# Kernel optimization log

Hardware: AMD Instinct MI355X
Metric: run time of the kernel (lower is better)

The kernel has to match this reference:

```python
import jax, jax.numpy as jnp
import numpy as np

N_NODES = 100000
N_EDGES = 800000
N_DIM = 2
HID = 128
EPS = 1e-12  # torch F.normalize eps


def setup_inputs() -> dict:
    key = jax.random.key(0)
    ks = jax.random.split(key, 12)
    x = jax.random.normal(ks[0], (N_NODES, N_DIM), dtype=jnp.float32)
    v = jax.random.normal(ks[1], (N_NODES, N_DIM), dtype=jnp.float32)
    src = jax.random.randint(ks[2], (N_EDGES,), 0, N_NODES, dtype=jnp.int32)
    dst = jax.random.randint(ks[3], (N_EDGES,), 0, N_NODES, dtype=jnp.int32)
    # fNN parameters, stored as [in, out] (y = h @ W + b, equivalent to torch Linear)
    def lin(k, fan_in, fan_out):
        bound = 1.0 / np.sqrt(fan_in)
        kw, kb = jax.random.split(k)
        W = jax.random.uniform(kw, (fan_in, fan_out), jnp.float32, -bound, bound)
        b = jax.random.uniform(kb, (fan_out,), jnp.float32, -bound, bound)
        return W, b
    W0, b0 = lin(ks[4], 1, HID)
    W1, b1 = lin(ks[5], HID, HID)
    W2, b2 = lin(ks[6], HID, HID)
    W3, b3 = lin(ks[7], HID, 1)
    gamma = jnp.float32(0.1)
    return {"x": x, "v": v, "src": src, "dst": dst, "gamma": gamma,
            "W0": W0, "b0": b0, "W1": W1, "b1": b1,
            "W2": W2, "b2": b2, "W3": W3, "b3": b3}


def reference(x, v, src, dst, gamma, W0, b0, W1, b1, W2, b2, W3, b3):
    n_nodes = x.shape[0]
    # per-edge displacement: dst position - src position (non-periodic euclid)
    dr = x[dst] - x[src]                                  # [E, N_dim]
    abs_dr = jnp.linalg.norm(dr, axis=-1, keepdims=True)  # [E, 1]
    unit_dr = dr / jnp.maximum(abs_dr, EPS)               # F.normalize
    # small MLP on scalar distance: 1 -> 128 -> 128 -> 128 -> 1, ReLU between
    h = jax.nn.relu(abs_dr @ W0 + b0)
    h = jax.nn.relu(h @ W1 + b1)
    h = jax.nn.relu(h @ W2 + b2)
    force = h @ W3 + b3                                   # [E, 1]
    msg = force * unit_dr                                 # [E, N_dim]
    # scatter-sum messages onto destination nodes
    sum_force = jax.ops.segment_sum(msg, dst, num_segments=n_nodes)  # [N, N_dim]
    # acceleration = aggregated force - gamma * velocity
    return sum_force - gamma * v
```

## Files before the change

kernel.cpp:

```cpp
#include <hip/hip_runtime.h>
#include <math.h>


#define M_TAB 4096
#define INV_MTAB (1.0f / 4096.0f)
#define EPSF 1e-12f
#define RANGE_N 2048
#define RSHIFT 11
#define NBUCK 64
#define P_SL 8
#define BCHUNK 2048
#define TPTS 8
#define NTABB (M_TAB / TPTS)
#define MAXRUN 64
#define SRC_BITS 17
#define SRC_MASK 0x1FFFFu

__device__ __forceinline__ void build_table8(
    int base, int tid, const float* __restrict__ W0,
    const float* __restrict__ b0, const float* __restrict__ W1,
    const float* __restrict__ b1, const float* __restrict__ W2,
    const float* __restrict__ b2, const float* __restrict__ W3,
    const float* __restrict__ b3, float* __restrict__ table,
    float* bufA, float* bufB) {
  const int j = tid;
  if (j < 128) {
    float w = W0[j], b = b0[j];
#pragma unroll
    for (int p = 0; p < TPTS; ++p) {
      float u = (float)(base + p) * INV_MTAB;
      float dd = u / (1.f - u);
      bufA[j * TPTS + p] = fmaxf(fmaf(dd, w, b), 0.f);
    }
  }
  __syncthreads();
  float acc[TPTS];
  if (j < 128) {
    float b = b1[j];
#pragma unroll
    for (int p = 0; p < TPTS; ++p) acc[p] = b;
#pragma unroll 8
    for (int k = 0; k < 128; ++k) {
      float w = W1[k * 128 + j];
      float4 h0 = *(const float4*)&bufA[k * TPTS];
      float4 h1 = *(const float4*)&bufA[k * TPTS + 4];
      acc[0] = fmaf(h0.x, w, acc[0]);
      acc[1] = fmaf(h0.y, w, acc[1]);
      acc[2] = fmaf(h0.z, w, acc[2]);
      acc[3] = fmaf(h0.w, w, acc[3]);
      acc[4] = fmaf(h1.x, w, acc[4]);
      acc[5] = fmaf(h1.y, w, acc[5]);
      acc[6] = fmaf(h1.z, w, acc[6]);
      acc[7] = fmaf(h1.w, w, acc[7]);
    }
  }
  __syncthreads();
  if (j < 128) {
#pragma unroll
    for (int p = 0; p < TPTS; ++p) bufB[j * TPTS + p] = fmaxf(acc[p], 0.f);
  }
  __syncthreads();
  if (j < 128) {
    float b = b2[j];
#pragma unroll
    for (int p = 0; p < TPTS; ++p) acc[p] = b;
#pragma unroll 8
    for (int k = 0; k < 128; ++k) {
      float w = W2[k * 128 + j];
      float4 h0 = *(const float4*)&bufB[k * TPTS];
      float4 h1 = *(const float4*)&bufB[k * TPTS + 4];
      acc[0] = fmaf(h0.x, w, acc[0]);
      acc[1] = fmaf(h0.y, w, acc[1]);
      acc[2] = fmaf(h0.z, w, acc[2]);
      acc[3] = fmaf(h0.w, w, acc[3]);
      acc[4] = fmaf(h1.x, w, acc[4]);
      acc[5] = fmaf(h1.y, w, acc[5]);
      acc[6] = fmaf(h1.z, w, acc[6]);
      acc[7] = fmaf(h1.w, w, acc[7]);
    }
    float w3 = W3[j];
#pragma unroll
    for (int p = 0; p < TPTS; ++p) bufA[j * TPTS + p] = fmaxf(acc[p], 0.f) * w3;
  }
  __syncthreads();
  for (int s = 64; s > 0; s >>= 1) {
    if (j < s) {
#pragma unroll
      for (int p = 0; p < TPTS; ++p)
        bufA[j * TPTS + p] += bufA[(j + s) * TPTS + p];
    }
    __syncthreads();
  }
  if (j < TPTS) table[base + j] = bufA[j] + b3[0];
}

__global__ __launch_bounds__(256) void kbin(
    const int* __restrict__ src, const int* __restrict__ dst,
    const float* __restrict__ W0, const float* __restrict__ b0,
    const float* __restrict__ W1, const float* __restrict__ b1,
    const float* __restrict__ W2, const float* __restrict__ b2,
    const float* __restrict__ W3, const float* __restrict__ b3,
    unsigned* __restrict__ binData, int* __restrict__ cntTab,
    int* __restrict__ offTab, float* __restrict__ table, int E, int NB) {
  __shared__ float smem[2048];
  __shared__ int cntL[NBUCK];
  __shared__ int offL[NBUCK];
  const int tid = threadIdx.x;
  const int bid = blockIdx.x;

  if (bid < NTABB) {
    build_table8(bid * TPTS, tid, W0, b0, W1, b1, W2, b2, W3, b3, table,
                 smem, smem + 1024);
    return;
  }
  const int b = bid - NTABB;
  if (tid < NBUCK) cntL[tid] = 0;
  __syncthreads();
  const int e0 = b * BCHUNK + tid * 8;
  int mdst[8], msrc[8], mrank[8];
  if (e0 + 7 < E) {
    int4 c0 = *(const int4*)(dst + e0);
    int4 c1 = *(const int4*)(dst + e0 + 4);
    int4 a0 = *(const int4*)(src + e0);
    int4 a1 = *(const int4*)(src + e0 + 4);
    mdst[0] = c0.x; mdst[1] = c0.y; mdst[2] = c0.z; mdst[3] = c0.w;
    mdst[4] = c1.x; mdst[5] = c1.y; mdst[6] = c1.z; mdst[7] = c1.w;
    msrc[0] = a0.x; msrc[1] = a0.y; msrc[2] = a0.z; msrc[3] = a0.w;
    msrc[4] = a1.x; msrc[5] = a1.y; msrc[6] = a1.z; msrc[7] = a1.w;
  } else {
#pragma unroll
    for (int i = 0; i < 8; ++i) {
      bool vv = (e0 + i < E);
      msrc[i] = vv ? src[e0 + i] : 0;
      mdst[i] = vv ? dst[e0 + i] : -1;
    }
  }
#pragma unroll
  for (int i = 0; i < 8; ++i)
    if (mdst[i] >= 0) mrank[i] = atomicAdd(&cntL[mdst[i] >> RSHIFT], 1);
  __syncthreads();
  if (tid == 0) {
    int s = 0;
#pragma unroll
    for (int k = 0; k < NBUCK; ++k) {
      offL[k] = s;
      s += cntL[k];
    }
  }
  __syncthreads();
  if (tid < NBUCK) {
    cntTab[b * NBUCK + tid] = cntL[tid];
    offTab[b * NBUCK + tid] = offL[tid];
  }
  unsigned* gout = binData + (size_t)b * BCHUNK;
#pragma unroll
  for (int i = 0; i < 8; ++i) {
    if (mdst[i] >= 0) {
      int pos = offL[mdst[i] >> RSHIFT] + mrank[i];
      gout[pos] = ((unsigned)(mdst[i] & (RANGE_N - 1)) << SRC_BITS) |
                  (unsigned)msrc[i];
    }
  }
}

__global__ __launch_bounds__(512) void kcons(
    const unsigned* __restrict__ binData, const int* __restrict__ cntTab,
    const int* __restrict__ offTab, const float* __restrict__ table,
    const float* __restrict__ x, float* __restrict__ partial, int NB,
    int n_nodes, int n_out) {
  __shared__ float acc[RANGE_N * 2];
  __shared__ float2 xl[RANGE_N];
  __shared__ int runStart[MAXRUN];
  __shared__ int pref[MAXRUN + 1];
  const int tid = threadIdx.x;
  const int p = blockIdx.x & (P_SL - 1);
  const int r = blockIdx.x >> 3;
  const int node0 = r * RANGE_N;

  for (int i = tid; i < RANGE_N * 2; i += 512) acc[i] = 0.f;
  for (int i = tid; i < RANGE_N; i += 512)
    xl[i] = (node0 + i < n_nodes) ? ((const float2*)x)[node0 + i]
                                  : make_float2(0.f, 0.f);
  const int nrun = (NB - p + P_SL - 1) / P_SL;
  for (int j = tid; j < nrun; j += 512) {
    int b = p + j * P_SL;
    runStart[j] = b * BCHUNK + offTab[b * NBUCK + r];
    pref[j + 1] = cntTab[b * NBUCK + r];
  }
  __syncthreads();
  if (tid == 0) {
    pref[0] = 0;
    for (int j = 0; j < nrun; ++j) pref[j + 1] += pref[j];
  }
  __syncthreads();

  const int T = pref[nrun];
  for (int g = tid; g < T; g += 512) {
    int lo = 0, hi = nrun;
    while (hi - lo > 1) {
      int mid = (lo + hi) >> 1;
      if (pref[mid] <= g) lo = mid; else hi = mid;
    }
    unsigned ent = binData[(size_t)runStart[lo] + (g - pref[lo])];
    int dloc = (int)(ent >> SRC_BITS);
    int s = (int)(ent & SRC_MASK);
    float2 xs = ((const float2*)x)[s];
    float2 xt = xl[dloc];
    float dx = xt.x - xs.x, dy = xt.y - xs.y;
    float d = sqrtf(fmaf(dx, dx, dy * dy));
    float u = d / (1.f + d);
    float idxf = u * (float)M_TAB;
    int i0 = (int)idxf;
    if (i0 > M_TAB - 2) i0 = M_TAB - 2;
    float frac = idxf - (float)i0;
    float f0 = table[i0], f1 = table[i0 + 1];
    float f = fmaf(frac, f1 - f0, f0);
    float sc = f / fmaxf(d, EPSF);
    atomicAdd(&acc[dloc * 2], sc * dx);
    atomicAdd(&acc[dloc * 2 + 1], sc * dy);
  }
  __syncthreads();

  const int cnt2 = min(RANGE_N, n_nodes - node0);
  float2* po = (float2*)(partial + (size_t)p * n_out) + node0;
  const float2* a2 = (const float2*)acc;
  for (int i = tid; i < cnt2; i += 512) po[i] = a2[i];
}

__global__ __launch_bounds__(256) void k4_finish(
    const float4* __restrict__ v4, const float* __restrict__ gamma,
    const float4* __restrict__ part4, float4* __restrict__ out4, int n4) {
  int i = blockIdx.x * blockDim.x + threadIdx.x;
  if (i >= n4) return;
  float g = -gamma[0];
  float4 a = v4[i];
  float4 acc = make_float4(g * a.x, g * a.y, g * a.z, g * a.w);
#pragma unroll
  for (int c = 0; c < P_SL; ++c) {
    float4 p = part4[(size_t)c * n4 + i];
    acc.x += p.x;
    acc.y += p.y;
    acc.z += p.z;
    acc.w += p.w;
  }
  out4[i] = acc;
}

__global__ __launch_bounds__(128) void k2_table(
    const float* __restrict__ W0, const float* __restrict__ b0,
    const float* __restrict__ W1, const float* __restrict__ b1,
    const float* __restrict__ W2, const float* __restrict__ b2,
    const float* __restrict__ W3, const float* __restrict__ b3,
    float* __restrict__ table) {
  __shared__ float bufA[1024];
  __shared__ float bufB[1024];
  build_table8(blockIdx.x * TPTS, threadIdx.x, W0, b0, W1, b1, W2, b2, W3,
               b3, table, bufA, bufB);
}

__global__ __launch_bounds__(256) void k0_init(const float* __restrict__ v,
                                               const float* __restrict__ gamma,
                                               float* __restrict__ out,
                                               int n) {
  int i = blockIdx.x * blockDim.x + threadIdx.x;
  if (i < n) out[i] = -gamma[0] * v[i];
}

__global__ __launch_bounds__(256) void k3_direct(
    const float* __restrict__ x, const int* __restrict__ src,
    const int* __restrict__ dst, const float* __restrict__ table,
    float* __restrict__ out, int E) {
  int e = blockIdx.x * blockDim.x + threadIdx.x;
  if (e >= E) return;
  int s = src[e], t = dst[e];
  float2 xs = ((const float2*)x)[s];
  float2 xt = ((const float2*)x)[t];
  float dx = xt.x - xs.x, dy = xt.y - xs.y;
  float d = sqrtf(fmaf(dx, dx, dy * dy));
  float u = d / (1.f + d);
  float idxf = u * (float)M_TAB;
  int i0 = (int)idxf;
  if (i0 > M_TAB - 2) i0 = M_TAB - 2;
  float frac = idxf - (float)i0;
  float f = fmaf(frac, table[i0 + 1] - table[i0], table[i0]);
  float sc = f / fmaxf(d, EPSF);
  atomicAdd(&out[2 * t + 0], sc * dx);
  atomicAdd(&out[2 * t + 1], sc * dy);
}

extern "C" void kernel_launch(void* const* d_in, const int* in_sizes, int n_in,
                              void* d_out, int out_size, void* d_ws,
                              size_t ws_size, hipStream_t stream) {
  const float* x = (const float*)d_in[0];
  const float* v = (const float*)d_in[1];
  const int* src = (const int*)d_in[2];
  const int* dst = (const int*)d_in[3];
  const float* gamma = (const float*)d_in[4];
  const float* W0 = (const float*)d_in[5];
  const float* b0 = (const float*)d_in[6];
  const float* W1 = (const float*)d_in[7];
  const float* b1 = (const float*)d_in[8];
  const float* W2 = (const float*)d_in[9];
  const float* b2 = (const float*)d_in[10];
  const float* W3 = (const float*)d_in[11];
  const float* b3 = (const float*)d_in[12];
  float* out = (float*)d_out;
  float* table = (float*)d_ws;

  int n_out = out_size;
  int n_nodes = in_sizes[0] / 2;
  int E = in_sizes[2];

  const int NB = (E + BCHUNK - 1) / BCHUNK;
  const int NR = (n_nodes + RANGE_N - 1) / RANGE_N;
  size_t sz_tab = ((size_t)NB * NBUCK * 4 + 255) & ~(size_t)255;
  size_t off_cnt = 65536;
  size_t off_off = off_cnt + sz_tab;
  size_t off_part = off_off + sz_tab;
  size_t off_bin = off_part + (size_t)P_SL * n_out * 4;
  size_t need = off_bin + (size_t)NB * BCHUNK * 4;

  bool fast = (ws_size >= need) && (n_out == 2 * n_nodes) &&
              (n_nodes <= (1 << SRC_BITS)) && (NR <= NBUCK) &&
              (NB <= P_SL * MAXRUN) && ((n_out & 3) == 0);

  if (fast) {
    int* cntTab = (int*)((char*)d_ws + off_cnt);
    int* offTab = (int*)((char*)d_ws + off_off);
    float* partial = (float*)((char*)d_ws + off_part);
    unsigned* binData = (unsigned*)((char*)d_ws + off_bin);
    hipLaunchKernelGGL(kbin, dim3(NTABB + NB), dim3(256), 0, stream, src, dst,
                       W0, b0, W1, b1, W2, b2, W3, b3, binData, cntTab,
                       offTab, table, E, NB);
    hipLaunchKernelGGL(kcons, dim3(NR * P_SL), dim3(512), 0, stream, binData,
                       cntTab, offTab, table, x, partial, NB, n_nodes, n_out);
    hipLaunchKernelGGL(k4_finish, dim3((n_out / 4 + 255) / 256), dim3(256), 0,
                       stream, (const float4*)v, gamma, (const float4*)partial,
                       (float4*)out, n_out / 4);
  } else {
    hipLaunchKernelGGL(k2_table, dim3(NTABB), dim3(128), 0, stream, W0, b0,
                       W1, b1, W2, b2, W3, b3, table);
    hipLaunchKernelGGL(k0_init, dim3((n_out + 255) / 256), dim3(256), 0,
                       stream, v, gamma, out, n_out);
    hipLaunchKernelGGL(k3_direct, dim3((E + 255) / 256), dim3(256), 0, stream,
                       x, src, dst, table, out, E);
  }
}
```

Before: 42.85 us.

## Use fine-grained node ranges with one consumer block each and fuse finish

Shrinks the destination range per bucket from 2048 to 256 nodes, giving 391 buckets. Each consumer block now owns one range and walks all edge chunks, which removes the 8-way partial slices and lets it write the final output (sum minus gamma times v) directly, so the separate finish kernel and partial buffers go away. Bucket prefix sums in both kernels become a two-level parallel scan to cope with the larger bucket and run counts. The cost is more per-chunk table entries to write and read, and each consumer block scans about 400 runs with a deeper binary search.

```diff
diff --git a/kernel.cpp b/kernel.cpp
--- a/kernel.cpp
+++ b/kernel.cpp
@@ -5,14 +5,13 @@
 #define M_TAB 4096
 #define INV_MTAB (1.0f / 4096.0f)
 #define EPSF 1e-12f
-#define RANGE_N 2048
-#define RSHIFT 11
-#define NBUCK 64
-#define P_SL 8
+#define RANGE_N 256
+#define RSHIFT 8
 #define BCHUNK 2048
 #define TPTS 8
 #define NTABB (M_TAB / TPTS)
-#define MAXRUN 64
+#define NB_MAX 400
+#define NBUCK_LIM 512
 #define SRC_BITS 17
 #define SRC_MASK 0x1FFFFu
 
@@ -101,10 +100,12 @@
     const float* __restrict__ W2, const float* __restrict__ b2,
     const float* __restrict__ W3, const float* __restrict__ b3,
     unsigned* __restrict__ binData, int* __restrict__ cntTab,
-    int* __restrict__ offTab, float* __restrict__ table, int E, int NB) {
+    int* __restrict__ offTab, float* __restrict__ table, int E, int NB,
+    int NBUCK) {
   __shared__ float smem[2048];
-  __shared__ int cntL[NBUCK];
-  __shared__ int offL[NBUCK];
+  __shared__ int cntL[NBUCK_LIM];
+  __shared__ int offL[NBUCK_LIM];
+  __shared__ int grp[64], gpre[64];
   const int tid = threadIdx.x;
   const int bid = blockIdx.x;
 
@@ -114,7 +115,7 @@
     return;
   }
   const int b = bid - NTABB;
-  if (tid < NBUCK) cntL[tid] = 0;
+  for (int i = tid; i < NBUCK; i += 256) cntL[i] = 0;
   __syncthreads();
   const int e0 = b * BCHUNK + tid * 8;
   int mdst[8], msrc[8], mrank[8];
@@ -139,18 +140,35 @@
   for (int i = 0; i < 8; ++i)
     if (mdst[i] >= 0) mrank[i] = atomicAdd(&cntL[mdst[i] >> RSHIFT], 1);
   __syncthreads();
+  const int NSEG = (NBUCK + 7) / 8;
+  if (tid < NSEG) {
+    int s = 0;
+    int k0 = tid * 8, k1 = min(NBUCK, k0 + 8);
+    for (int k = k0; k < k1; ++k) {
+      int c = cntL[k];
+      offL[k] = s;
+      s += c;
+    }
+    grp[tid] = s;
+  }
+  __syncthreads();
   if (tid == 0) {
     int s = 0;
-#pragma unroll
-    for (int k = 0; k < NBUCK; ++k) {
-      offL[k] = s;
-      s += cntL[k];
-    }
-  }
-  __syncthreads();
-  if (tid < NBUCK) {
-    cntTab[b * NBUCK + tid] = cntL[tid];
-    offTab[b * NBUCK + tid] = offL[tid];
+    for (int t = 0; t < NSEG; ++t) {
+      gpre[t] = s;
+      s += grp[t];
+    }
+  }
+  __syncthreads();
+  if (tid < NSEG) {
+    int g0 = gpre[tid];
+    int k0 = tid * 8, k1 = min(NBUCK, k0 + 8);
+    for (int k = k0; k < k1; ++k) offL[k] += g0;
+  }
+  __syncthreads();
+  for (int i = tid; i < NBUCK; i += 256) {
+    cntTab[b * NBUCK + i] = cntL[i];
+    offTab[b * NBUCK + i] = offL[i];
   }
   unsigned* gout = binData + (size_t)b * BCHUNK;
 #pragma unroll
@@ -166,37 +184,57 @@
 __global__ __launch_bounds__(512) void kcons(
     const unsigned* __restrict__ binData, const int* __restrict__ cntTab,
     const int* __restrict__ offTab, const float* __restrict__ table,
-    const float* __restrict__ x, float* __restrict__ partial, int NB,
-    int n_nodes, int n_out) {
+    const float* __restrict__ x, const float* __restrict__ v,
+    const float* __restrict__ gamma, float* __restrict__ out, int NB,
+    int NBUCK, int n_nodes) {
   __shared__ float acc[RANGE_N * 2];
   __shared__ float2 xl[RANGE_N];
-  __shared__ int runStart[MAXRUN];
-  __shared__ int pref[MAXRUN + 1];
+  __shared__ int runStart[NB_MAX];
+  __shared__ int pref[NB_MAX + 1];
+  __shared__ int grp[64], gpre[64];
   const int tid = threadIdx.x;
-  const int p = blockIdx.x & (P_SL - 1);
-  const int r = blockIdx.x >> 3;
+  const int r = blockIdx.x;
   const int node0 = r * RANGE_N;
 
   for (int i = tid; i < RANGE_N * 2; i += 512) acc[i] = 0.f;
   for (int i = tid; i < RANGE_N; i += 512)
     xl[i] = (node0 + i < n_nodes) ? ((const float2*)x)[node0 + i]
                                   : make_float2(0.f, 0.f);
-  const int nrun = (NB - p + P_SL - 1) / P_SL;
-  for (int j = tid; j < nrun; j += 512) {
-    int b = p + j * P_SL;
-    runStart[j] = b * BCHUNK + offTab[b * NBUCK + r];
-    pref[j + 1] = cntTab[b * NBUCK + r];
+  for (int j = tid; j < NB; j += 512) {
+    runStart[j] = j * BCHUNK + offTab[j * NBUCK + r];
+    pref[j + 1] = cntTab[j * NBUCK + r];
+  }
+  if (tid == 0) pref[0] = 0;
+  __syncthreads();
+  const int NSEG = (NB + 7) / 8;
+  if (tid < NSEG) {
+    int s = 0;
+    int k0 = tid * 8, k1 = min(NB, k0 + 8);
+    for (int k = k0; k < k1; ++k) {
+      s += pref[k + 1];
+      pref[k + 1] = s;
+    }
+    grp[tid] = s;
   }
   __syncthreads();
   if (tid == 0) {
-    pref[0] = 0;
-    for (int j = 0; j < nrun; ++j) pref[j + 1] += pref[j];
-  }
-  __syncthreads();
-
-  const int T = pref[nrun];
+    int s = 0;
+    for (int t = 0; t < NSEG; ++t) {
+      gpre[t] = s;
+      s += grp[t];
+    }
+  }
+  __syncthreads();
+  if (tid < NSEG) {
+    int g0 = gpre[tid];
+    int k0 = tid * 8, k1 = min(NB, k0 + 8);
+    for (int k = k0; k < k1; ++k) pref[k + 1] += g0;
+  }
+  __syncthreads();
+
+  const int T = pref[NB];
   for (int g = tid; g < T; g += 512) {
-    int lo = 0, hi = nrun;
+    int lo = 0, hi = NB;
     while (hi - lo > 1) {
       int mid = (lo + hi) >> 1;
       if (pref[mid] <= g) lo = mid; else hi = mid;
@@ -222,28 +260,15 @@
   __syncthreads();
 
   const int cnt2 = min(RANGE_N, n_nodes - node0);
-  float2* po = (float2*)(partial + (size_t)p * n_out) + node0;
+  const float gm = -gamma[0];
+  float2* po = (float2*)out + node0;
+  const float2* pv = (const float2*)v + node0;
   const float2* a2 = (const float2*)acc;
-  for (int i = tid; i < cnt2; i += 512) po[i] = a2[i];
-}
-
-__global__ __launch_bounds__(256) void k4_finish(
-    const float4* __restrict__ v4, const float* __restrict__ gamma,
-    const float4* __restrict__ part4, float4* __restrict__ out4, int n4) {
-  int i = blockIdx.x * blockDim.x + threadIdx.x;
-  if (i >= n4) return;
-  float g = -gamma[0];
-  float4 a = v4[i];
-  float4 acc = make_float4(g * a.x, g * a.y, g * a.z, g * a.w);
-#pragma unroll
-  for (int c = 0; c < P_SL; ++c) {
-    float4 p = part4[(size_t)c * n4 + i];
-    acc.x += p.x;
-    acc.y += p.y;
-    acc.z += p.z;
-    acc.w += p.w;
-  }
-  out4[i] = acc;
+  for (int i = tid; i < cnt2; i += 512) {
+    float2 a = a2[i];
+    float2 vv = pv[i];
+    po[i] = make_float2(fmaf(gm, vv.x, a.x), fmaf(gm, vv.y, a.y));
+  }
 }
 
 __global__ __launch_bounds__(128) void k2_table(
@@ -312,31 +337,27 @@
   int E = in_sizes[2];
 
   const int NB = (E + BCHUNK - 1) / BCHUNK;
-  const int NR = (n_nodes + RANGE_N - 1) / RANGE_N;
+  const int NBUCK = (n_nodes + RANGE_N - 1) / RANGE_N;
   size_t sz_tab = ((size_t)NB * NBUCK * 4 + 255) & ~(size_t)255;
   size_t off_cnt = 65536;
   size_t off_off = off_cnt + sz_tab;
-  size_t off_part = off_off + sz_tab;
-  size_t off_bin = off_part + (size_t)P_SL * n_out * 4;
+  size_t off_bin = off_off + sz_tab;
   size_t need = off_bin + (size_t)NB * BCHUNK * 4;
 
   bool fast = (ws_size >= need) && (n_out == 2 * n_nodes) &&
-              (n_nodes <= (1 << SRC_BITS)) && (NR <= NBUCK) &&
-              (NB <= P_SL * MAXRUN) && ((n_out & 3) == 0);
+              (n_nodes <= (1 << SRC_BITS)) && (NBUCK <= NBUCK_LIM) &&
+              (NB <= NB_MAX);
 
   if (fast) {
     int* cntTab = (int*)((char*)d_ws + off_cnt);
     int* offTab = (int*)((char*)d_ws + off_off);
-    float* partial = (float*)((char*)d_ws + off_part);
     unsigned* binData = (unsigned*)((char*)d_ws + off_bin);
     hipLaunchKernelGGL(kbin, dim3(NTABB + NB), dim3(256), 0, stream, src, dst,
                        W0, b0, W1, b1, W2, b2, W3, b3, binData, cntTab,
-                       offTab, table, E, NB);
-    hipLaunchKernelGGL(kcons, dim3(NR * P_SL), dim3(512), 0, stream, binData,
-                       cntTab, offTab, table, x, partial, NB, n_nodes, n_out);
-    hipLaunchKernelGGL(k4_finish, dim3((n_out / 4 + 255) / 256), dim3(256), 0,
-                       stream, (const float4*)v, gamma, (const float4*)partial,
-                       (float4*)out, n_out / 4);
+                       offTab, table, E, NB, NBUCK);
+    hipLaunchKernelGGL(kcons, dim3(NBUCK), dim3(512), 0, stream, binData,
+                       cntTab, offTab, table, x, v, gamma, out, NB, NBUCK,
+                       n_nodes);
   } else {
     hipLaunchKernelGGL(k2_table, dim3(NTABB), dim3(128), 0, stream, W0, b0,
                        W1, b1, W2, b2, W3, b3, table);
```

Measured after the change: 47.92 us. 11.8% more time.
